# Kernel tuning notes

Measured on AMD Instinct MI355X. Metric: run time of the kernel, lower is better.

Reference implementation:

```python
import jax, jax.numpy as jnp
import numpy as np

S, B, D, H = 512, 128, 512, 256


def setup_inputs() -> dict:
    key = jax.random.key(0)
    ks = jax.random.split(key, 6)
    inputs = jax.random.normal(ks[0], (S, B, D), dtype=jnp.float32)
    # Parent-pointer trees: parent[b, i] in (i, S-1]; node S-1 is the root,
    # whose 'parent' is the sentinel slot S (its contributions are discarded).
    rng = np.random.default_rng(0)
    off = rng.integers(1, S, size=(B, S))
    par = np.minimum(np.arange(S)[None, :] + off, S - 1)
    par[:, S - 1] = S  # root sentinel
    parents = jnp.asarray(par, dtype=jnp.int32)
    s_in = 1.0 / np.sqrt(D)
    s_h = 1.0 / np.sqrt(H)
    W_iou = (jax.random.normal(ks[1], (D, 3 * H), dtype=jnp.float32) * s_in)
    b_iou = jnp.zeros((3 * H,), jnp.float32)
    U_iou = (jax.random.normal(ks[2], (H, 3 * H), dtype=jnp.float32) * s_h)
    W_f = (jax.random.normal(ks[3], (D, H), dtype=jnp.float32) * s_in)
    b_f = jnp.zeros((H,), jnp.float32)
    U_f = (jax.random.normal(ks[4], (H, H), dtype=jnp.float32) * s_h)
    return {"inputs": inputs, "parents": parents, "W_iou": W_iou, "b_iou": b_iou,
            "U_iou": U_iou, "W_f": W_f, "b_f": b_f, "U_f": U_f}


def reference(inputs, parents, W_iou, b_iou, U_iou, W_f, b_f, U_f):
    S_, B_, D_ = inputs.shape
    H_ = U_f.shape[0]
    # Precompute input projections for all nodes (one big GEMM each).
    x_iou = jnp.einsum('sbd,dg->sbg', inputs, W_iou) + b_iou          # [S,B,3H]
    x_f = jnp.einsum('sbd,dh->sbh', inputs, W_f) + b_f                # [S,B,H]
    x_f_pad = jnp.concatenate([x_f, jnp.zeros((1, B_, H_), x_f.dtype)], axis=0)  # sentinel row
    bidx = jnp.arange(B_)

    def step(carry, xs):
        hsum, fcsum = carry                 # [B, S+1, H]: per-node child-h sum / sum_k f_k*c_k
        xi, p, idx = xs                     # xi [B,3H], p [B] parent index, idx node index
        ht = hsum[:, idx]                   # sum of children h for node idx
        fct = fcsum[:, idx]                 # sum of f_k * c_k over children
        g = xi + ht @ U_iou                 # [B,3H]
        i_g = jax.nn.sigmoid(g[:, :H_])
        o_g = jax.nn.sigmoid(g[:, H_:2 * H_])
        u_g = jnp.tanh(g[:, 2 * H_:])
        c = i_g * u_g + fct
        h = o_g * jnp.tanh(c)
        # per-child forget gate, computed against the parent's input projection
        f = jax.nn.sigmoid(x_f_pad[p, bidx] + h @ U_f)                # [B,H]
        hsum = hsum.at[bidx, p].add(h)
        fcsum = fcsum.at[bidx, p].add(f * c)
        return (hsum, fcsum), (h, c)

    zeros = jnp.zeros((B_, S_ + 1, H_), inputs.dtype)
    xs = (x_iou, parents.T, jnp.arange(S_))
    _, (hs, _cs) = jax.lax.scan(step, (zeros, zeros), xs)
    contexts = hs                            # [seq, batch, H] (all node hidden states)
    root_h = hs[-1][None]                    # [1, batch, H]   (root hidden state)
    return contexts, root_h
```

## Files before the change

kernel.cpp:

```cpp
#include <hip/hip_runtime.h>
#include <hip/hip_bf16.h>
#include <cstdint>
#include <cstddef>

#define DI __device__ __forceinline__
#define RLX __ATOMIC_RELAXED
#define AGT __HIP_MEMORY_SCOPE_AGENT
#define WGP __HIP_MEMORY_SCOPE_WORKGROUP

typedef __attribute__((ext_vector_type(8))) short          bf16x8;
typedef __attribute__((ext_vector_type(8))) unsigned short u16x8;
typedef __attribute__((ext_vector_type(4))) float          f32x4;

constexpr int Sv = 512, Bv = 128, Dv = 512, Hv = 256;

constexpr size_t SZ_FCSUM  = (size_t)128 * 513 * 256 * 4;
constexpr size_t OFF_FCSUM = 0;
constexpr size_t OFF_HX    = SZ_FCSUM;
constexpr size_t SZ_HX     = (size_t)511 * 128 * 256 * 4;
constexpr size_t OFF_GSUM  = OFF_HX + SZ_HX;
constexpr size_t SZ_GSUM   = (size_t)128 * 513 * 768 * 4;
constexpr size_t OFF_XF    = OFF_GSUM + SZ_GSUM;
constexpr size_t SZ_XF     = (size_t)512 * 128 * 256 * 4;
constexpr size_t OFF_BTH   = OFF_XF + SZ_XF;
constexpr size_t OFF_BTL   = OFF_BTH + (size_t)1024 * 512 * 2;
constexpr size_t OFF_UH    = OFF_BTL + (size_t)1024 * 512 * 2;
constexpr size_t OFF_UL    = OFF_UH + (size_t)1024 * 256 * 2;

DI unsigned short f2bf(float x) {
  union { float f; uint32_t u; } v; v.f = x;
  uint32_t r = v.u + 0x7fffu + ((v.u >> 16) & 1u);
  return (unsigned short)(r >> 16);
}
DI float bf2f(unsigned short b) {
  union { uint32_t u; float f; } v; v.u = ((uint32_t)b) << 16; return v.f;
}
DI float sigm(float x) { return 1.0f / (1.0f + __expf(-x)); }
DI bool okd(unsigned d) { return (d & 0x7F800000u) != 0x7F800000u; }
DI bool ok64(unsigned long long v) { return okd((unsigned)v) && okd((unsigned)(v >> 32)); }

__global__ void cvt_w_kernel(const float* __restrict__ Wiou, const float* __restrict__ Wf,
                             unsigned short* __restrict__ bth, unsigned short* __restrict__ btl)
{
  int idx = blockIdx.x * 256 + threadIdx.x;
  int n = idx >> 9, k = idx & 511;
  float v = (n < 768) ? Wiou[(size_t)k * 768 + n] : Wf[(size_t)k * 256 + (n - 768)];
  unsigned short h = f2bf(v);
  bth[idx] = h;
  btl[idx] = f2bf(v - bf2f(h));
}

__global__ void cvt_u_kernel(const float* __restrict__ Uiou, const float* __restrict__ Uf,
                             unsigned short* __restrict__ uh, unsigned short* __restrict__ ul)
{
  int idx = blockIdx.x * 256 + threadIdx.x;
  int col = idx >> 8, k = idx & 255;
  float v = (col < 768) ? Uiou[(size_t)k * 768 + col] : Uf[(size_t)k * 256 + (col - 768)];
  unsigned short h = f2bf(v);
  uh[idx] = h;
  ul[idx] = f2bf(v - bf2f(h));
}

#define GLD_LDS16(gp, lp) __builtin_amdgcn_global_load_lds( \
    (const __attribute__((address_space(1))) unsigned int*)(gp), \
    (__attribute__((address_space(3))) unsigned int*)(lp), 16, 0, 0)

__global__ __launch_bounds__(256, 2)
void gemm_split_kernel(const float* __restrict__ A,
                       const unsigned short* __restrict__ BTh,
                       const unsigned short* __restrict__ BTl,
                       const float* __restrict__ biou, const float* __restrict__ bfv,
                       float* __restrict__ gsum, float* __restrict__ xf)
{
  extern __shared__ char lds[];
  unsigned short* As = (unsigned short*)lds;
  unsigned short* Bs = (unsigned short*)(lds + 32768);

  const int bid = blockIdx.x;
  const int ntile = bid & 7, mtile = bid >> 3;
  const int m0 = mtile * 128, n0 = ntile * 128;
  const int tid = threadIdx.x;
  const int lane = tid & 63, w = tid >> 6;
  const int wr = w >> 1, wc = w & 1;

  f32x4 acc[4][4];
  #pragma unroll
  for (int i = 0; i < 4; i++)
    #pragma unroll
    for (int jj = 0; jj < 4; jj++) acc[i][jj] = f32x4{0.f, 0.f, 0.f, 0.f};

  const int arow = tid >> 1, ahalf = tid & 1;
  float areg[32];

  auto issueA = [&](int kk0) {
    const float* g = A + (size_t)(m0 + arow) * 512 + kk0 + ahalf * 32;
    #pragma unroll
    for (int i = 0; i < 8; i++) {
      f32x4 v = ((const f32x4*)g)[i];
      areg[i * 4 + 0] = v[0]; areg[i * 4 + 1] = v[1];
      areg[i * 4 + 2] = v[2]; areg[i * 4 + 3] = v[3];
    }
  };
  auto writeA = [&](int buf, int low) {
    unsigned short* dst = As + buf * 8192 + arow * 64 + ahalf * 32;
    #pragma unroll
    for (int i = 0; i < 4; i++) {
      u16x8 o;
      #pragma unroll
      for (int jj = 0; jj < 8; jj++) {
        float x = areg[i * 8 + jj];
        unsigned short h = f2bf(x);
        o[jj] = low ? f2bf(x - bf2f(h)) : h;
      }
      *(u16x8*)(dst + i * 8) = o;
    }
  };
  auto stageB = [&](int buf, const unsigned short* Bbase, int kk0) {
    #pragma unroll
    for (int q = 0; q < 4; q++) {
      int cidx = q * 256 + tid;
      int row = cidx >> 3, blk = cidx & 7;
      const unsigned short* g = Bbase + (size_t)(n0 + row) * 512 + kk0 + blk * 8;
      unsigned short* l = Bs + buf * 8192 + cidx * 8;
      GLD_LDS16(g, l);
    }
  };
  auto alow = [](int t) { return ((t >> 3) == 1) ? 1 : 0; };

  issueA(0);
  stageB(0, BTh, 0);
  asm volatile("s_waitcnt vmcnt(0)" ::: "memory");
  writeA(0, alow(0));
  __syncthreads();

  for (int t = 0; t < 24; ++t) {
    const int buf = t & 1;
    if (t < 23) {
      const int tn = t + 1;
      issueA((tn & 7) * 64);
      stageB(buf ^ 1, (tn < 16) ? BTh : BTl, (tn & 7) * 64);
    }
    #pragma unroll
    for (int kk = 0; kk < 64; kk += 32) {
      const int k8 = (lane >> 4) * 8;
      bf16x8 af[4], bfrag[4];
      #pragma unroll
      for (int mi = 0; mi < 4; ++mi)
        af[mi] = *(const bf16x8*)(As + buf * 8192 + (size_t)(wr * 64 + mi * 16 + (lane & 15)) * 64 + kk + k8);
      #pragma unroll
      for (int ni = 0; ni < 4; ++ni)
        bfrag[ni] = *(const bf16x8*)(Bs + buf * 8192 + (size_t)(wc * 64 + ni * 16 + (lane & 15)) * 64 + kk + k8);
      #pragma unroll
      for (int mi = 0; mi < 4; ++mi)
        #pragma unroll
        for (int ni = 0; ni < 4; ++ni)
          acc[mi][ni] = __builtin_amdgcn_mfma_f32_16x16x32_bf16(af[mi], bfrag[ni], acc[mi][ni], 0, 0, 0);
    }
    if (t < 23) {
      asm volatile("s_waitcnt vmcnt(0)" ::: "memory");
      writeA(buf ^ 1, alow(t + 1));
    }
    __syncthreads();
  }

  const bool isiou = (n0 < 768);
  const int s_ = mtile;
  #pragma unroll
  for (int ni = 0; ni < 4; ++ni) {
    int coln = n0 + wc * 64 + ni * 16 + (lane & 15);
    float bv = isiou ? biou[coln] : bfv[coln - 768];
    #pragma unroll
    for (int mi = 0; mi < 4; ++mi)
      #pragma unroll
      for (int r = 0; r < 4; ++r) {
        int bg = wr * 64 + mi * 16 + (lane >> 4) * 4 + r;
        float v = acc[mi][ni][r] + bv;
        if (isiou) gsum[((size_t)bg * 513 + s_) * 768 + coln] = v;
        else       xf[((size_t)s_ * 128 + bg) * 256 + (coln - 768)] = v;
      }
  }
}

__global__ __launch_bounds__(512, 1)
void scan_kernel(const unsigned short* __restrict__ ubh, const unsigned short* __restrict__ ubl,
                 const float* __restrict__ xf, const int* __restrict__ parents,
                 float* gsum, float* fcsum, unsigned* hx,
                 float* __restrict__ out)
{
  __shared__ __align__(16) unsigned short AH[8 * 64 * 8];
  __shared__ __align__(16) unsigned short AL[8 * 64 * 8];
  __shared__ float gcor[16 * 96];
  __shared__ float fcor[16 * 32];
  __shared__ float cbuf[16 * 32];
  __shared__ int   pbuf[2][16];
  __shared__ int   pl[16];

  const int bid = blockIdx.x;
  const int g = bid & 7, j = bid >> 3;
  const int tid = threadIdx.x;
  const int lane = tid & 63, w = tid >> 6;
  const int gb = g * 16;

  const int colb = (w >> 1) * 256 + j * 32 + (w & 1) * 16;
  const int bcol = colb + (lane & 15);
  const int bk8 = (lane >> 4) * 8;
  bf16x8 BH[8], BL[8];
  #pragma unroll
  for (int kc = 0; kc < 8; ++kc) {
    BH[kc] = *(const bf16x8*)(ubh + (size_t)bcol * 256 + kc * 32 + bk8);
    BL[kc] = *(const bf16x8*)(ubl + (size_t)bcol * 256 + kc * 32 + bk8);
  }

  const int skc = tid >> 6, sl = tid & 63;
  const int sb = sl & 15, sk0 = skc * 32 + (sl >> 4) * 8;
  const int ab = tid >> 5, ahc = tid & 31;
  const int abs_b = gb + ab, acol = j * 32 + ahc;
  const bool isf = (w >= 6);
  const int fr0 = (lane >> 4) * 4;
  const int fcl = (w & 1) * 16 + (lane & 15);

  if (tid < 16) { pbuf[0][tid] = parents[(gb + tid) * 512]; pl[tid] = -1; }

  float pre_i, pre_o, pre_u, fct_pre;
  {
    size_t gi0 = ((size_t)abs_b * 513) * 768 + acol;
    pre_i = gsum[gi0];
    pre_o = gsum[gi0 + 256];
    pre_u = gsum[gi0 + 512];
    fct_pre = fcsum[((size_t)abs_b * 513) * 256 + acol];
  }
  float xfv[4] = {0.f, 0.f, 0.f, 0.f};
  __syncthreads();

  #pragma unroll 1
  for (int s = 0; s < 512; ++s) {
    if (s > 0) {
      const unsigned long long* s64 =
          (const unsigned long long*)(hx + ((size_t)(s - 1) * 8 + g) * 4096 + sb * 256 + sk0);
      unsigned long long v0, v1, v2, v3;
      for (;;) {
        v0 = __hip_atomic_load(s64 + 0, RLX, AGT);
        v1 = __hip_atomic_load(s64 + 1, RLX, AGT);
        v2 = __hip_atomic_load(s64 + 2, RLX, AGT);
        v3 = __hip_atomic_load(s64 + 3, RLX, AGT);
        if (ok64(v0) && ok64(v1) && ok64(v2) && ok64(v3)) break;
      }
      u16x8 hiv, lov;
      unsigned long long vv[4] = {v0, v1, v2, v3};
      #pragma unroll
      for (int q = 0; q < 4; ++q) {
        unsigned lo32 = (unsigned)vv[q], hi32 = (unsigned)(vv[q] >> 32);
        hiv[2 * q]     = (unsigned short)(lo32 >> 16);
        lov[2 * q]     = (unsigned short)(lo32 & 0xffffu);
        hiv[2 * q + 1] = (unsigned short)(hi32 >> 16);
        lov[2 * q + 1] = (unsigned short)(hi32 & 0xffffu);
      }
      *(u16x8*)(AH + skc * 512 + sl * 8) = hiv;
      *(u16x8*)(AL + skc * 512 + sl * 8) = lov;
    }
    __syncthreads();

    if (s > 0) {
      f32x4 a0 = {0.f, 0.f, 0.f, 0.f};
      f32x4 a1 = {0.f, 0.f, 0.f, 0.f};
      f32x4 a2 = {0.f, 0.f, 0.f, 0.f};
      #pragma unroll
      for (int kc = 0; kc < 8; ++kc) {
        bf16x8 ah = *(const bf16x8*)(AH + kc * 512 + lane * 8);
        bf16x8 al = *(const bf16x8*)(AL + kc * 512 + lane * 8);
        a0 = __builtin_amdgcn_mfma_f32_16x16x32_bf16(ah, BH[kc], a0, 0, 0, 0);
        a1 = __builtin_amdgcn_mfma_f32_16x16x32_bf16(al, BH[kc], a1, 0, 0, 0);
        a2 = __builtin_amdgcn_mfma_f32_16x16x32_bf16(ah, BL[kc], a2, 0, 0, 0);
      }
      f32x4 acc = a0 + a1 + a2;
      if (!isf) {
        const int colg = colb + (lane & 15);
        const int colL = (w >> 1) * 32 + (w & 1) * 16 + (lane & 15);
        #pragma unroll
        for (int r = 0; r < 4; ++r) {
          int rb = fr0 + r;
          int p = pbuf[(s - 1) & 1][rb];
          if (p == s) gcor[rb * 96 + colL] = acc[r];
          else __hip_atomic_fetch_add(&gsum[((size_t)(gb + rb) * 513 + p) * 768 + colg],
                                      acc[r], RLX, WGP);
        }
      } else {
        #pragma unroll
        for (int r = 0; r < 4; ++r) {
          int rb = fr0 + r;
          int p = pbuf[(s - 1) & 1][rb];
          float fg = sigm(xfv[r] + acc[r]);
          float fc = fg * cbuf[rb * 32 + fcl];
          if (p == s) fcor[rb * 32 + fcl] = fc;
          else __hip_atomic_fetch_add(&fcsum[((size_t)(gb + rb) * 513 + p) * 256 + j * 32 + fcl],
                                      fc, RLX, WGP);
        }
        if (w == 6 && (lane & 15) == 0) {
          #pragma unroll
          for (int r = 0; r < 4; ++r) pl[fr0 + r] = pbuf[(s - 1) & 1][fr0 + r];
        }
      }
    }

    asm volatile("s_waitcnt vmcnt(0)" ::: "memory");
    __syncthreads();

    {
      bool corr = (pl[ab] == s);
      float gi = pre_i + (corr ? gcor[ab * 96 + ahc] : 0.f);
      float go = pre_o + (corr ? gcor[ab * 96 + 32 + ahc] : 0.f);
      float gu = pre_u + (corr ? gcor[ab * 96 + 64 + ahc] : 0.f);
      float fct = fct_pre + (corr ? fcor[ab * 32 + ahc] : 0.f);
      float c = sigm(gi) * tanhf(gu) + fct;
      float h = sigm(go) * tanhf(c);
      if (s < 511) {
        unsigned short hh = f2bf(h);
        unsigned short hl = f2bf(h - bf2f(hh));
        unsigned packed = ((unsigned)hh << 16) | hl;
        __hip_atomic_store(&hx[((size_t)s * 8 + g) * 4096 + ab * 256 + acol],
                           packed, RLX, AGT);
      }
      cbuf[ab * 32 + ahc] = c;
      out[((size_t)s * 128 + abs_b) * 256 + acol] = h;
      if (s == 511) out[(size_t)512 * 128 * 256 + (size_t)abs_b * 256 + acol] = h;
    }

    if (s < 511) {
      const int sn = s + 1;
      {
        size_t gi1 = ((size_t)abs_b * 513 + sn) * 768 + acol;
        pre_i = gsum[gi1];
        pre_o = gsum[gi1 + 256];
        pre_u = gsum[gi1 + 512];
        fct_pre = fcsum[((size_t)abs_b * 513 + sn) * 256 + acol];
      }
      if (tid < 16) pbuf[sn & 1][tid] = parents[(gb + tid) * 512 + sn];
      if (isf) {
        #pragma unroll
        for (int r = 0; r < 4; ++r) {
          int p = pbuf[s & 1][fr0 + r];
          xfv[r] = (p < 512) ? xf[((size_t)p * 128 + (gb + fr0 + r)) * 256 + j * 32 + fcl] : 0.f;
        }
      }
    }
  }
}

extern "C" void kernel_launch(void* const* d_in, const int* in_sizes, int n_in,
                              void* d_out, int out_size, void* d_ws, size_t ws_size,
                              hipStream_t stream)
{
  (void)in_sizes; (void)n_in; (void)out_size; (void)ws_size;
  const float* inputs  = (const float*)d_in[0];
  const int*   parents = (const int*)d_in[1];
  const float* Wiou    = (const float*)d_in[2];
  const float* biou    = (const float*)d_in[3];
  const float* Uiou    = (const float*)d_in[4];
  const float* Wf      = (const float*)d_in[5];
  const float* bf_     = (const float*)d_in[6];
  const float* Uf      = (const float*)d_in[7];
  float* out = (float*)d_out;
  char* ws = (char*)d_ws;

  float* fcsum = (float*)(ws + OFF_FCSUM);
  unsigned* hx = (unsigned*)(ws + OFF_HX);
  float* gsum  = (float*)(ws + OFF_GSUM);
  float* xf    = (float*)(ws + OFF_XF);
  unsigned short* bth = (unsigned short*)(ws + OFF_BTH);
  unsigned short* btl = (unsigned short*)(ws + OFF_BTL);
  unsigned short* uh  = (unsigned short*)(ws + OFF_UH);
  unsigned short* ul  = (unsigned short*)(ws + OFF_UL);

  hipMemsetAsync(ws + OFF_FCSUM, 0, SZ_FCSUM, stream);
  hipMemsetAsync(ws + OFF_HX, 0xFF, SZ_HX, stream);

  hipFuncSetAttribute((const void*)gemm_split_kernel,
                      hipFuncAttributeMaxDynamicSharedMemorySize, 65536);

  cvt_w_kernel<<<2048, 256, 0, stream>>>(Wiou, Wf, bth, btl);
  cvt_u_kernel<<<1024, 256, 0, stream>>>(Uiou, Uf, uh, ul);
  gemm_split_kernel<<<4096, 256, 65536, stream>>>(inputs, bth, btl, biou, bf_, gsum, xf);
  scan_kernel<<<64, 512, 0, stream>>>(uh, ul, xf, parents, gsum, fcsum, hx, out);
}
```

Baseline: 2.427 ms.

## Restructure scan step: register parents, double-buffered s+1 corrections, bypass loads, fast tanh

Parent indices are now read straight into registers per step instead of being staged through shared pbuf and pl arrays. Contributions to node s+1 go into a double-buffered shared correction buffer rather than global atomics, which removes the race between atomics and the next step's prefetch of gsum. The spin-wait on the previous step's h now uses wide cache-bypassing dwordx4 loads with a wave-wide __all check, and tanhf is replaced by a clamped exp-based tanh. In exchange, the gsum, fcsum and xf prefetch now happens at the start of each step instead of overlapping the previous step's tail, which puts those loads on the critical path.

```diff
diff --git a/kernel.cpp b/kernel.cpp
--- a/kernel.cpp
+++ b/kernel.cpp
@@ -11,6 +11,7 @@
 typedef __attribute__((ext_vector_type(8))) short          bf16x8;
 typedef __attribute__((ext_vector_type(8))) unsigned short u16x8;
 typedef __attribute__((ext_vector_type(4))) float          f32x4;
+typedef __attribute__((ext_vector_type(4))) unsigned int   u32x4;
 
 constexpr int Sv = 512, Bv = 128, Dv = 512, Hv = 256;
 
@@ -36,8 +37,12 @@
   union { uint32_t u; float f; } v; v.u = ((uint32_t)b) << 16; return v.f;
 }
 DI float sigm(float x) { return 1.0f / (1.0f + __expf(-x)); }
+DI float tanh_fast(float x) {
+  float xc = fminf(fmaxf(x, -9.0f), 9.0f);
+  float e = __expf(2.0f * xc);
+  return (e - 1.0f) / (e + 1.0f);
+}
 DI bool okd(unsigned d) { return (d & 0x7F800000u) != 0x7F800000u; }
-DI bool ok64(unsigned long long v) { return okd((unsigned)v) && okd((unsigned)(v >> 32)); }
 
 __global__ void cvt_w_kernel(const float* __restrict__ Wiou, const float* __restrict__ Wf,
                              unsigned short* __restrict__ bth, unsigned short* __restrict__ btl)
@@ -189,11 +194,11 @@
 {
   __shared__ __align__(16) unsigned short AH[8 * 64 * 8];
   __shared__ __align__(16) unsigned short AL[8 * 64 * 8];
-  __shared__ float gcor[16 * 96];
-  __shared__ float fcor[16 * 32];
+  __shared__ float gcorA[16 * 96];
+  __shared__ float gcorB[2][16 * 96];
+  __shared__ float fcorA[16 * 32];
+  __shared__ float fcorB[2][16 * 32];
   __shared__ float cbuf[16 * 32];
-  __shared__ int   pbuf[2][16];
-  __shared__ int   pl[16];
 
   const int bid = blockIdx.x;
   const int g = bid & 7, j = bid >> 3;
@@ -218,42 +223,59 @@
   const bool isf = (w >= 6);
   const int fr0 = (lane >> 4) * 4;
   const int fcl = (w & 1) * 16 + (lane & 15);
-
-  if (tid < 16) { pbuf[0][tid] = parents[(gb + tid) * 512]; pl[tid] = -1; }
-
-  float pre_i, pre_o, pre_u, fct_pre;
-  {
-    size_t gi0 = ((size_t)abs_b * 513) * 768 + acol;
-    pre_i = gsum[gi0];
-    pre_o = gsum[gi0 + 256];
-    pre_u = gsum[gi0 + 512];
-    fct_pre = fcsum[((size_t)abs_b * 513) * 256 + acol];
-  }
-  float xfv[4] = {0.f, 0.f, 0.f, 0.f};
+  const int colL = (w >> 1) * 32 + (w & 1) * 16 + (lane & 15);
+  const int colg = colb + (lane & 15);
+
   __syncthreads();
 
   #pragma unroll 1
   for (int s = 0; s < 512; ++s) {
+    asm volatile("s_waitcnt vmcnt(0)" ::: "memory");
+
+    float pre_i, pre_o, pre_u, fct_pre;
+    {
+      size_t gi = ((size_t)abs_b * 513 + s) * 768 + acol;
+      pre_i = gsum[gi]; pre_o = gsum[gi + 256]; pre_u = gsum[gi + 512];
+      fct_pre = fcsum[((size_t)abs_b * 513 + s) * 256 + acol];
+    }
+    int pr[4] = {0, 0, 0, 0};
+    float xfv[4] = {0.f, 0.f, 0.f, 0.f};
     if (s > 0) {
-      const unsigned long long* s64 =
-          (const unsigned long long*)(hx + ((size_t)(s - 1) * 8 + g) * 4096 + sb * 256 + sk0);
-      unsigned long long v0, v1, v2, v3;
+      #pragma unroll
+      for (int r = 0; r < 4; ++r)
+        pr[r] = parents[(gb + fr0 + r) * 512 + (s - 1)];
+      if (isf) {
+        #pragma unroll
+        for (int r = 0; r < 4; ++r)
+          xfv[r] = (pr[r] < 512)
+                 ? xf[((size_t)pr[r] * 128 + (gb + fr0 + r)) * 256 + j * 32 + fcl] : 0.f;
+      }
+    }
+    const int pa1 = (s > 0) ? parents[abs_b * 512 + (s - 1)] : -1;
+    const int pa2 = (s > 1) ? parents[abs_b * 512 + (s - 2)] : -1;
+
+    if (s > 0) {
+      const unsigned* src = hx + ((size_t)(s - 1) * 8 + g) * 4096 + sb * 256 + sk0;
+      u32x4 r0, r1;
       for (;;) {
-        v0 = __hip_atomic_load(s64 + 0, RLX, AGT);
-        v1 = __hip_atomic_load(s64 + 1, RLX, AGT);
-        v2 = __hip_atomic_load(s64 + 2, RLX, AGT);
-        v3 = __hip_atomic_load(s64 + 3, RLX, AGT);
-        if (ok64(v0) && ok64(v1) && ok64(v2) && ok64(v3)) break;
+        asm volatile("global_load_dwordx4 %0, %2, off sc0 sc1\n\t"
+                     "global_load_dwordx4 %1, %3, off sc0 sc1\n\t"
+                     "s_waitcnt vmcnt(0)"
+                     : "=&v"(r0), "=&v"(r1)
+                     : "v"(src), "v"(src + 4)
+                     : "memory");
+        bool ok = true;
+        #pragma unroll
+        for (int q = 0; q < 4; ++q) ok = ok && okd(r0[q]) && okd(r1[q]);
+        if (__all(ok)) break;
       }
       u16x8 hiv, lov;
-      unsigned long long vv[4] = {v0, v1, v2, v3};
       #pragma unroll
       for (int q = 0; q < 4; ++q) {
-        unsigned lo32 = (unsigned)vv[q], hi32 = (unsigned)(vv[q] >> 32);
-        hiv[2 * q]     = (unsigned short)(lo32 >> 16);
-        lov[2 * q]     = (unsigned short)(lo32 & 0xffffu);
-        hiv[2 * q + 1] = (unsigned short)(hi32 >> 16);
-        lov[2 * q + 1] = (unsigned short)(hi32 & 0xffffu);
+        hiv[q]     = (unsigned short)(r0[q] >> 16);
+        lov[q]     = (unsigned short)(r0[q] & 0xffffu);
+        hiv[4 + q] = (unsigned short)(r1[q] >> 16);
+        lov[4 + q] = (unsigned short)(r1[q] & 0xffffu);
       }
       *(u16x8*)(AH + skc * 512 + sl * 8) = hiv;
       *(u16x8*)(AL + skc * 512 + sl * 8) = lov;
@@ -274,45 +296,43 @@
       }
       f32x4 acc = a0 + a1 + a2;
       if (!isf) {
-        const int colg = colb + (lane & 15);
-        const int colL = (w >> 1) * 32 + (w & 1) * 16 + (lane & 15);
         #pragma unroll
         for (int r = 0; r < 4; ++r) {
-          int rb = fr0 + r;
-          int p = pbuf[(s - 1) & 1][rb];
-          if (p == s) gcor[rb * 96 + colL] = acc[r];
+          int rb = fr0 + r, p = pr[r];
+          if (p == s)          gcorA[rb * 96 + colL] = acc[r];
+          else if (p == s + 1) gcorB[s & 1][rb * 96 + colL] = acc[r];
           else __hip_atomic_fetch_add(&gsum[((size_t)(gb + rb) * 513 + p) * 768 + colg],
                                       acc[r], RLX, WGP);
         }
       } else {
         #pragma unroll
         for (int r = 0; r < 4; ++r) {
-          int rb = fr0 + r;
-          int p = pbuf[(s - 1) & 1][rb];
+          int rb = fr0 + r, p = pr[r];
           float fg = sigm(xfv[r] + acc[r]);
           float fc = fg * cbuf[rb * 32 + fcl];
-          if (p == s) fcor[rb * 32 + fcl] = fc;
+          if (p == s)          fcorA[rb * 32 + fcl] = fc;
+          else if (p == s + 1) fcorB[s & 1][rb * 32 + fcl] = fc;
           else __hip_atomic_fetch_add(&fcsum[((size_t)(gb + rb) * 513 + p) * 256 + j * 32 + fcl],
                                       fc, RLX, WGP);
         }
-        if (w == 6 && (lane & 15) == 0) {
-          #pragma unroll
-          for (int r = 0; r < 4; ++r) pl[fr0 + r] = pbuf[(s - 1) & 1][fr0 + r];
-        }
-      }
-    }
-
-    asm volatile("s_waitcnt vmcnt(0)" ::: "memory");
+      }
+    }
     __syncthreads();
 
     {
-      bool corr = (pl[ab] == s);
-      float gi = pre_i + (corr ? gcor[ab * 96 + ahc] : 0.f);
-      float go = pre_o + (corr ? gcor[ab * 96 + 32 + ahc] : 0.f);
-      float gu = pre_u + (corr ? gcor[ab * 96 + 64 + ahc] : 0.f);
-      float fct = fct_pre + (corr ? fcor[ab * 32 + ahc] : 0.f);
-      float c = sigm(gi) * tanhf(gu) + fct;
-      float h = sigm(go) * tanhf(c);
+      const bool cA = (pa1 == s);
+      const bool cB = (pa2 == s);
+      const int pb = (s - 1) & 1;
+      float gi = pre_i + (cA ? gcorA[ab * 96 + ahc] : 0.f)
+                       + (cB ? gcorB[pb][ab * 96 + ahc] : 0.f);
+      float go = pre_o + (cA ? gcorA[ab * 96 + 32 + ahc] : 0.f)
+                       + (cB ? gcorB[pb][ab * 96 + 32 + ahc] : 0.f);
+      float gu = pre_u + (cA ? gcorA[ab * 96 + 64 + ahc] : 0.f)
+                       + (cB ? gcorB[pb][ab * 96 + 64 + ahc] : 0.f);
+      float fct = fct_pre + (cA ? fcorA[ab * 32 + ahc] : 0.f)
+                          + (cB ? fcorB[pb][ab * 32 + ahc] : 0.f);
+      float c = sigm(gi) * tanh_fast(gu) + fct;
+      float h = sigm(go) * tanh_fast(c);
       if (s < 511) {
         unsigned short hh = f2bf(h);
         unsigned short hl = f2bf(h - bf2f(hh));
@@ -323,25 +343,6 @@
       cbuf[ab * 32 + ahc] = c;
       out[((size_t)s * 128 + abs_b) * 256 + acol] = h;
       if (s == 511) out[(size_t)512 * 128 * 256 + (size_t)abs_b * 256 + acol] = h;
-    }
-
-    if (s < 511) {
-      const int sn = s + 1;
-      {
-        size_t gi1 = ((size_t)abs_b * 513 + sn) * 768 + acol;
-        pre_i = gsum[gi1];
-        pre_o = gsum[gi1 + 256];
-        pre_u = gsum[gi1 + 512];
-        fct_pre = fcsum[((size_t)abs_b * 513 + sn) * 256 + acol];
-      }
-      if (tid < 16) pbuf[sn & 1][tid] = parents[(gb + tid) * 512 + sn];
-      if (isf) {
-        #pragma unroll
-        for (int r = 0; r < 4; ++r) {
-          int p = pbuf[s & 1][fr0 + r];
-          xfv[r] = (p < 512) ? xf[((size_t)p * 128 + (gb + fr0 + r)) * 256 + j * 32 + fcl] : 0.f;
-        }
-      }
     }
   }
 }
```

Measured after the change: 2.736 ms. +12.7%, slower.

## Pre-split inputs to bf16 hi/lo and stage A via direct LDS loads

Applied to the files above, without the earlier changes.

Adds a kernel that converts the fp32 input activations into bf16 high and low halves once, stored in workspace that aliases the fcsum/hx region (the memsets are moved after the GEMM). The GEMM then stages A with global_load_lds exactly as it stages B, removing register round-trips and per-tile conversion that were repeated for each of the 8 column tiles. It also replaces tanhf with an exp-based clamped tanh in the scan cell. The cost is an extra pass writing 128MB of bf16 data, and slightly different tanh accuracy.

```diff
diff --git a/kernel.cpp b/kernel.cpp
--- a/kernel.cpp
+++ b/kernel.cpp
@@ -10,6 +10,7 @@
 
 typedef __attribute__((ext_vector_type(8))) short          bf16x8;
 typedef __attribute__((ext_vector_type(8))) unsigned short u16x8;
+typedef __attribute__((ext_vector_type(4))) unsigned short u16x4;
 typedef __attribute__((ext_vector_type(4))) float          f32x4;
 
 constexpr int Sv = 512, Bv = 128, Dv = 512, Hv = 256;
@@ -26,6 +27,9 @@
 constexpr size_t OFF_BTL   = OFF_BTH + (size_t)1024 * 512 * 2;
 constexpr size_t OFF_UH    = OFF_BTL + (size_t)1024 * 512 * 2;
 constexpr size_t OFF_UL    = OFF_UH + (size_t)1024 * 256 * 2;
+constexpr size_t OFF_ATH   = 0;
+constexpr size_t SZ_ATH    = (size_t)65536 * 512 * 2;
+constexpr size_t OFF_ATL   = OFF_ATH + SZ_ATH;
 
 DI unsigned short f2bf(float x) {
   union { float f; uint32_t u; } v; v.f = x;
@@ -36,6 +40,11 @@
   union { uint32_t u; float f; } v; v.u = ((uint32_t)b) << 16; return v.f;
 }
 DI float sigm(float x) { return 1.0f / (1.0f + __expf(-x)); }
+DI float tanh_fast(float x) {
+  float xc = fminf(fmaxf(x, -9.0f), 9.0f);
+  float e = __expf(2.0f * xc);
+  return (e - 1.0f) / (e + 1.0f);
+}
 DI bool okd(unsigned d) { return (d & 0x7F800000u) != 0x7F800000u; }
 DI bool ok64(unsigned long long v) { return okd((unsigned)v) && okd((unsigned)(v >> 32)); }
 
@@ -61,12 +70,28 @@
   ul[idx] = f2bf(v - bf2f(h));
 }
 
+__global__ void cvt_a_kernel(const float* __restrict__ A,
+                             unsigned short* __restrict__ ath, unsigned short* __restrict__ atl)
+{
+  int idx = blockIdx.x * 256 + threadIdx.x;
+  f32x4 v = ((const f32x4*)A)[idx];
+  u16x4 h, l;
+  #pragma unroll
+  for (int q = 0; q < 4; ++q) {
+    h[q] = f2bf(v[q]);
+    l[q] = f2bf(v[q] - bf2f(h[q]));
+  }
+  ((u16x4*)ath)[idx] = h;
+  ((u16x4*)atl)[idx] = l;
+}
+
 #define GLD_LDS16(gp, lp) __builtin_amdgcn_global_load_lds( \
     (const __attribute__((address_space(1))) unsigned int*)(gp), \
     (__attribute__((address_space(3))) unsigned int*)(lp), 16, 0, 0)
 
 __global__ __launch_bounds__(256, 2)
-void gemm_split_kernel(const float* __restrict__ A,
+void gemm_split_kernel(const unsigned short* __restrict__ ATh,
+                       const unsigned short* __restrict__ ATl,
                        const unsigned short* __restrict__ BTh,
                        const unsigned short* __restrict__ BTl,
                        const float* __restrict__ biou, const float* __restrict__ bfv,
@@ -89,56 +114,29 @@
     #pragma unroll
     for (int jj = 0; jj < 4; jj++) acc[i][jj] = f32x4{0.f, 0.f, 0.f, 0.f};
 
-  const int arow = tid >> 1, ahalf = tid & 1;
-  float areg[32];
-
-  auto issueA = [&](int kk0) {
-    const float* g = A + (size_t)(m0 + arow) * 512 + kk0 + ahalf * 32;
+  auto stage = [&](unsigned short* dstbase, const unsigned short* src0,
+                   int row0, int kk0, int buf) {
     #pragma unroll
-    for (int i = 0; i < 8; i++) {
-      f32x4 v = ((const f32x4*)g)[i];
-      areg[i * 4 + 0] = v[0]; areg[i * 4 + 1] = v[1];
-      areg[i * 4 + 2] = v[2]; areg[i * 4 + 3] = v[3];
-    }
-  };
-  auto writeA = [&](int buf, int low) {
-    unsigned short* dst = As + buf * 8192 + arow * 64 + ahalf * 32;
-    #pragma unroll
-    for (int i = 0; i < 4; i++) {
-      u16x8 o;
-      #pragma unroll
-      for (int jj = 0; jj < 8; jj++) {
-        float x = areg[i * 8 + jj];
-        unsigned short h = f2bf(x);
-        o[jj] = low ? f2bf(x - bf2f(h)) : h;
-      }
-      *(u16x8*)(dst + i * 8) = o;
-    }
-  };
-  auto stageB = [&](int buf, const unsigned short* Bbase, int kk0) {
-    #pragma unroll
-    for (int q = 0; q < 4; q++) {
+    for (int q = 0; q < 4; ++q) {
       int cidx = q * 256 + tid;
       int row = cidx >> 3, blk = cidx & 7;
-      const unsigned short* g = Bbase + (size_t)(n0 + row) * 512 + kk0 + blk * 8;
-      unsigned short* l = Bs + buf * 8192 + cidx * 8;
-      GLD_LDS16(g, l);
+      const unsigned short* gp = src0 + (size_t)(row0 + row) * 512 + kk0 + blk * 8;
+      unsigned short* lp = dstbase + buf * 8192 + cidx * 8;
+      GLD_LDS16(gp, lp);
     }
   };
-  auto alow = [](int t) { return ((t >> 3) == 1) ? 1 : 0; };
-
-  issueA(0);
-  stageB(0, BTh, 0);
+
+  stage(As, ATh, m0, 0, 0);
+  stage(Bs, BTh, n0, 0, 0);
   asm volatile("s_waitcnt vmcnt(0)" ::: "memory");
-  writeA(0, alow(0));
   __syncthreads();
 
   for (int t = 0; t < 24; ++t) {
     const int buf = t & 1;
     if (t < 23) {
       const int tn = t + 1;
-      issueA((tn & 7) * 64);
-      stageB(buf ^ 1, (tn < 16) ? BTh : BTl, (tn & 7) * 64);
+      stage(As, (tn >= 8 && tn < 16) ? ATl : ATh, m0, (tn & 7) * 64, buf ^ 1);
+      stage(Bs, (tn < 16) ? BTh : BTl, n0, (tn & 7) * 64, buf ^ 1);
     }
     #pragma unroll
     for (int kk = 0; kk < 64; kk += 32) {
@@ -156,10 +154,7 @@
         for (int ni = 0; ni < 4; ++ni)
           acc[mi][ni] = __builtin_amdgcn_mfma_f32_16x16x32_bf16(af[mi], bfrag[ni], acc[mi][ni], 0, 0, 0);
     }
-    if (t < 23) {
-      asm volatile("s_waitcnt vmcnt(0)" ::: "memory");
-      writeA(buf ^ 1, alow(t + 1));
-    }
+    asm volatile("s_waitcnt vmcnt(0)" ::: "memory");
     __syncthreads();
   }
 
@@ -311,8 +306,8 @@
       float go = pre_o + (corr ? gcor[ab * 96 + 32 + ahc] : 0.f);
       float gu = pre_u + (corr ? gcor[ab * 96 + 64 + ahc] : 0.f);
       float fct = fct_pre + (corr ? fcor[ab * 32 + ahc] : 0.f);
-      float c = sigm(gi) * tanhf(gu) + fct;
-      float h = sigm(go) * tanhf(c);
+      float c = sigm(gi) * tanh_fast(gu) + fct;
+      float h = sigm(go) * tanh_fast(c);
       if (s < 511) {
         unsigned short hh = f2bf(h);
         unsigned short hl = f2bf(h - bf2f(hh));
@@ -370,15 +365,17 @@
   unsigned short* btl = (unsigned short*)(ws + OFF_BTL);
   unsigned short* uh  = (unsigned short*)(ws + OFF_UH);
   unsigned short* ul  = (unsigned short*)(ws + OFF_UL);
-
+  unsigned short* ath = (unsigned short*)(ws + OFF_ATH);
+  unsigned short* atl = (unsigned short*)(ws + OFF_ATL);
+
+  hipFuncSetAttribute((const void*)gemm_split_kernel,
+                      hipFuncAttributeMaxDynamicSharedMemorySize, 65536);
+
+  cvt_w_kernel<<<2048, 256, 0, stream>>>(Wiou, Wf, bth, btl);
+  cvt_u_kernel<<<1024, 256, 0, stream>>>(Uiou, Uf, uh, ul);
+  cvt_a_kernel<<<32768, 256, 0, stream>>>(inputs, ath, atl);
+  gemm_split_kernel<<<4096, 256, 65536, stream>>>(ath, atl, bth, btl, biou, bf_, gsum, xf);
   hipMemsetAsync(ws + OFF_FCSUM, 0, SZ_FCSUM, stream);
   hipMemsetAsync(ws + OFF_HX, 0xFF, SZ_HX, stream);
-
-  hipFuncSetAttribute((const void*)gemm_split_kernel,
-                      hipFuncAttributeMaxDynamicSharedMemorySize, 65536);
-
-  cvt_w_kernel<<<2048, 256, 0, stream>>>(Wiou, Wf, bth, btl);
-  cvt_u_kernel<<<1024, 256, 0, stream>>>(Uiou, Uf, uh, ul);
-  gemm_split_kernel<<<4096, 256, 65536, stream>>>(inputs, bth, btl, biou, bf_, gsum, xf);
   scan_kernel<<<64, 512, 0, stream>>>(uh, ul, xf, parents, gsum, fcsum, hx, out);
 }
```

Result: faster. 2.063 ms (-15.0%).
